# Optimization experiments

Measured on AMD Instinct MI355X. Metric: run time of the kernel, lower is better.

## Reference

```python
import jax, jax.numpy as jnp
import numpy as np

NEG_FILL = -100.0  # matches torch new_full(-100.0) init for scatter-amax


def reference(x, part_labels, parts_num=16):
    # x: (n, c, s, h, w) float; part_labels: (n, s, h, w) int in [0, parts_num)
    n, c, s, h, w = x.shape
    hw = h * w
    ns = n * s
    # (n s) c (h w)
    feat = jnp.transpose(x, (0, 2, 1, 3, 4)).reshape(ns, c, hw)
    labels = part_labels.reshape(ns, hw).astype(jnp.int32)

    b3 = jnp.arange(ns)[:, None, None]          # (ns,1,1)
    ch = jnp.arange(c)[None, :, None]            # (1,c,1)
    lbl3 = labels[:, None, :]                    # (ns,1,hw) -> broadcasts to (ns,c,hw)

    pooled_sum = jnp.zeros((ns, c, parts_num), x.dtype).at[b3, ch, lbl3].add(feat)
    b2 = jnp.arange(ns)[:, None]
    pooled_count = jnp.zeros((ns, parts_num), x.dtype).at[b2, labels].add(1.0)  # (ns,P)
    pooled_max = jnp.full((ns, c, parts_num), NEG_FILL, x.dtype).at[b3, ch, lbl3].max(feat)

    count = pooled_count[:, None, :]             # (ns,1,P)
    pooled_mean = pooled_sum / jnp.maximum(count, 1.0)
    pooled_max = jnp.where(count > 0, pooled_max, 0.0)
    pooled = pooled_mean + pooled_max            # (ns,c,P)
    # (n s) c p -> n c s p
    return jnp.transpose(pooled.reshape(n, s, c, parts_num), (0, 2, 1, 3))


def setup_inputs() -> dict:
    key = jax.random.key(0)
    k1, k2 = jax.random.split(key)
    n, c, s, h, w = 16, 256, 32, 16, 11
    parts_num = 16
    x = jax.random.normal(k1, (n, c, s, h, w), dtype=jnp.float32)
    part_labels = jax.random.randint(k2, (n, s, h, w), 0, parts_num, dtype=jnp.int64)
    return {"x": x, "part_labels": part_labels, "parts_num": parts_num}
```

## Files before the change

### kernel.cpp

```cpp
#include <hip/hip_runtime.h>


constexpr int C   = 256;
constexpr int S   = 32;
constexpr int HW  = 176;
constexpr int P   = 16;
constexpr int ROW = S * HW;
constexpr int GC  = 16;
constexpr int PITCH = 178;
constexpr int BCAP  = 64;
constexpr float NEG_FILL = -100.0f;

__device__ __forceinline__ void barrier_lgkm() {
    asm volatile("s_waitcnt lgkmcnt(0)\n\ts_barrier" ::: "memory");
}

__global__ __launch_bounds__(256) void hpp_kernel(
    const float* __restrict__ x,
    const int*   __restrict__ labels,
    float*       __restrict__ out)
{
    __shared__ float         tile[GC * PITCH];
    __shared__ unsigned char perm[P * BCAP];
    __shared__ int           cnt[P];

    const int tid = threadIdx.x;
    const int blk = blockIdx.x;
    const int ns  = blk >> 4, cg = blk & 15;
    const int n   = ns >> 5,  s  = ns & 31;

    const int* ln = labels + (size_t)ns * HW;
    int lab = 0;
    if (tid < HW) lab = ln[tid];

    const float* xb = x + (size_t)(n * C + cg * GC) * ROW + s * HW;
    const int f0 = tid, f1 = tid + 256, f2 = tid + 512;
    const int r0 = f0 / 44, j0 = f0 - r0 * 44;
    const int r1 = f1 / 44, j1 = f1 - r1 * 44;
    const int r2 = f2 / 44, j2 = f2 - r2 * 44;
    float4 v0 = *(const float4*)(xb + (size_t)r0 * ROW + j0 * 4);
    float4 v1 = *(const float4*)(xb + (size_t)r1 * ROW + j1 * 4);
    float4 v2 = make_float4(0.f, 0.f, 0.f, 0.f);
    const bool has2 = (f2 < GC * 44);
    if (has2) v2 = *(const float4*)(xb + (size_t)r2 * ROW + j2 * 4);

    ((unsigned*)perm)[tid] = 0u;
    if (tid < P) cnt[tid] = 0;
    barrier_lgkm();
    if (tid < HW) {
        int r = atomicAdd(&cnt[lab], 1);
        if (r < BCAP) perm[(lab << 6) + r] = (unsigned char)tid;
    }
    barrier_lgkm();

    {
        float2* t0 = (float2*)&tile[r0 * PITCH + j0 * 4];
        t0[0] = make_float2(v0.x, v0.y); t0[1] = make_float2(v0.z, v0.w);
        float2* t1 = (float2*)&tile[r1 * PITCH + j1 * 4];
        t1[0] = make_float2(v1.x, v1.y); t1[1] = make_float2(v1.z, v1.w);
        if (has2) {
            float2* t2 = (float2*)&tile[r2 * PITCH + j2 * 4];
            t2[0] = make_float2(v2.x, v2.y); t2[1] = make_float2(v2.z, v2.w);
        }
    }
    barrier_lgkm();

    const int p = tid >> 4, c = tid & 15;
    const int k = min(cnt[p], BCAP);
    const unsigned char* pp = &perm[p << 6];
    const float*         tc = &tile[c * PITCH];

    float s0 = 0.f, s1 = 0.f, m0 = NEG_FILL, m1 = NEG_FILL;
    const int kf = k & ~3;
    for (int j = 0; j < kf; j += 4) {
        unsigned u = *(const unsigned*)&pp[j];
        float a0 = tc[u & 0xFF];
        float a1 = tc[(u >> 8) & 0xFF];
        float a2 = tc[(u >> 16) & 0xFF];
        float a3 = tc[u >> 24];
        s0 += a0; m0 = fmaxf(m0, a0);
        s1 += a1; m1 = fmaxf(m1, a1);
        s0 += a2; m0 = fmaxf(m0, a2);
        s1 += a3; m1 = fmaxf(m1, a3);
    }
    if (kf < k) {
        unsigned u = *(const unsigned*)&pp[kf];
        float a0 = tc[u & 0xFF];
        float a1 = tc[(u >> 8) & 0xFF];
        float a2 = tc[(u >> 16) & 0xFF];
        s0 += a0; m0 = fmaxf(m0, a0);
        if (kf + 1 < k) { s1 += a1; m1 = fmaxf(m1, a1); }
        if (kf + 2 < k) { s0 += a2; m0 = fmaxf(m0, a2); }
    }

    float res = (k > 0) ? (s0 + s1) / (float)k + fmaxf(m0, m1) : 0.f;
    out[((size_t)(n * C + cg * GC + c) * S + s) * P + p] = res;
}

extern "C" void kernel_launch(void* const* d_in, const int* in_sizes, int n_in,
                              void* d_out, int out_size, void* d_ws, size_t ws_size,
                              hipStream_t stream) {
    const float* x      = (const float*)d_in[0];
    const int*   labels = (const int*)d_in[1];
    float*       out    = (float*)d_out;

    const int ns_total = in_sizes[1] / HW;
    const int nblk     = ns_total * (C / GC);
    hpp_kernel<<<nblk, 256, 0, stream>>>(x, labels, out);
}
```

Before: 135.5 us.

## Process two adjacent s slices per block with half the channels

Each block now covers 8 channels across two consecutive s positions instead of 16 channels at one s. Each channel's global read becomes a 352-float contiguous run, giving longer coalesced bursts, and two label rows are bucketed per block. The price is extra index arithmetic and a second set of part buckets in shared memory.

```diff
diff --git a/kernel.cpp b/kernel.cpp
--- a/kernel.cpp
+++ b/kernel.cpp
@@ -6,9 +6,11 @@
 constexpr int HW  = 176;
 constexpr int P   = 16;
 constexpr int ROW = S * HW;
-constexpr int GC  = 16;
+constexpr int GC  = 8;
+constexpr int NS2 = 2;
 constexpr int PITCH = 178;
 constexpr int BCAP  = 64;
+constexpr int PPITCH = 68;
 constexpr float NEG_FILL = -100.0f;
 
 __device__ __forceinline__ void barrier_lgkm() {
@@ -20,55 +22,65 @@
     const int*   __restrict__ labels,
     float*       __restrict__ out)
 {
-    __shared__ float         tile[GC * PITCH];
-    __shared__ unsigned char perm[P * BCAP];
-    __shared__ int           cnt[P];
+    __shared__ float         tile[GC * NS2 * PITCH];
+    __shared__ unsigned char perm[NS2 * P * PPITCH];
+    __shared__ int           cnt[NS2 * P];
 
     const int tid = threadIdx.x;
     const int blk = blockIdx.x;
-    const int ns  = blk >> 4, cg = blk & 15;
-    const int n   = ns >> 5,  s  = ns & 31;
+    const int nsp = blk >> 5, cg = blk & 31;
+    const int n   = nsp >> 4, sp = nsp & 15;
+    const int s   = sp * 2;
 
-    const int* ln = labels + (size_t)ns * HW;
-    int lab = 0;
-    if (tid < HW) lab = ln[tid];
+    const int* ln = labels + (size_t)(n * S + s) * HW;
+    int lab0 = 0, lab1 = 0;
+    if (tid < HW) { lab0 = ln[tid]; lab1 = ln[HW + tid]; }
 
     const float* xb = x + (size_t)(n * C + cg * GC) * ROW + s * HW;
     const int f0 = tid, f1 = tid + 256, f2 = tid + 512;
-    const int r0 = f0 / 44, j0 = f0 - r0 * 44;
-    const int r1 = f1 / 44, j1 = f1 - r1 * 44;
-    const int r2 = f2 / 44, j2 = f2 - r2 * 44;
+    const int r0 = f0 / 88, j0 = f0 - r0 * 88;
+    const int r1 = f1 / 88, j1 = f1 - r1 * 88;
+    const int r2 = f2 / 88, j2 = f2 - r2 * 88;
     float4 v0 = *(const float4*)(xb + (size_t)r0 * ROW + j0 * 4);
     float4 v1 = *(const float4*)(xb + (size_t)r1 * ROW + j1 * 4);
     float4 v2 = make_float4(0.f, 0.f, 0.f, 0.f);
-    const bool has2 = (f2 < GC * 44);
+    const bool has2 = (f2 < GC * 88);
     if (has2) v2 = *(const float4*)(xb + (size_t)r2 * ROW + j2 * 4);
 
-    ((unsigned*)perm)[tid] = 0u;
-    if (tid < P) cnt[tid] = 0;
+    if (tid < NS2 * P) cnt[tid] = 0;
     barrier_lgkm();
     if (tid < HW) {
-        int r = atomicAdd(&cnt[lab], 1);
-        if (r < BCAP) perm[(lab << 6) + r] = (unsigned char)tid;
+        int a = atomicAdd(&cnt[lab0], 1);
+        if (a < BCAP) perm[lab0 * PPITCH + a] = (unsigned char)tid;
+        int b = atomicAdd(&cnt[P + lab1], 1);
+        if (b < BCAP) perm[P * PPITCH + lab1 * PPITCH + b] = (unsigned char)tid;
     }
     barrier_lgkm();
 
     {
-        float2* t0 = (float2*)&tile[r0 * PITCH + j0 * 4];
+        const int q0 = j0 * 4, s20 = (q0 >= HW), h0 = q0 - s20 * HW;
+        float2* t0 = (float2*)&tile[(r0 * 2 + s20) * PITCH + h0];
         t0[0] = make_float2(v0.x, v0.y); t0[1] = make_float2(v0.z, v0.w);
-        float2* t1 = (float2*)&tile[r1 * PITCH + j1 * 4];
+
+        const int q1 = j1 * 4, s21 = (q1 >= HW), h1 = q1 - s21 * HW;
+        float2* t1 = (float2*)&tile[(r1 * 2 + s21) * PITCH + h1];
         t1[0] = make_float2(v1.x, v1.y); t1[1] = make_float2(v1.z, v1.w);
+
         if (has2) {
-            float2* t2 = (float2*)&tile[r2 * PITCH + j2 * 4];
+            const int q2 = j2 * 4, s22 = (q2 >= HW), h2 = q2 - s22 * HW;
+            float2* t2 = (float2*)&tile[(r2 * 2 + s22) * PITCH + h2];
             t2[0] = make_float2(v2.x, v2.y); t2[1] = make_float2(v2.z, v2.w);
         }
     }
     barrier_lgkm();
 
-    const int p = tid >> 4, c = tid & 15;
-    const int k = min(cnt[p], BCAP);
-    const unsigned char* pp = &perm[p << 6];
-    const float*         tc = &tile[c * PITCH];
+    const int p   = tid >> 4;
+    const int low = tid & 15;
+    const int sp2 = low & 1;
+    const int c   = low >> 1;
+    const int k   = min(cnt[sp2 * P + p], BCAP);
+    const unsigned char* pp = &perm[(sp2 * P + p) * PPITCH];
+    const float*         tc = &tile[low * PITCH];
 
     float s0 = 0.f, s1 = 0.f, m0 = NEG_FILL, m1 = NEG_FILL;
     const int kf = k & ~3;
@@ -94,7 +106,7 @@
     }
 
     float res = (k > 0) ? (s0 + s1) / (float)k + fmaxf(m0, m1) : 0.f;
-    out[((size_t)(n * C + cg * GC + c) * S + s) * P + p] = res;
+    out[((size_t)(n * C + cg * GC + c) * S + (s + sp2)) * P + p] = res;
 }
 
 extern "C" void kernel_launch(void* const* d_in, const int* in_sizes, int n_in,
@@ -105,6 +117,6 @@
     float*       out    = (float*)d_out;
 
     const int ns_total = in_sizes[1] / HW;
-    const int nblk     = ns_total * (C / GC);
+    const int nblk     = (ns_total / NS2) * (C / GC);
     hpp_kernel<<<nblk, 256, 0, stream>>>(x, labels, out);
 }
```

New measurement: 136.1 us. About the same (+0.5%).

## Precompute label buckets in a separate kernel and scatter x into part-sorted tiles

Applied to the files above, without the earlier changes.

Adds a bucket kernel that computes, for each (n,s) frame, each pixel's position in part-sorted order, plus per-part base offsets and counts, and writes these to workspace. The main kernel now handles one (n,c) row with all 32 frames. It scatters the loaded float4s into shared memory in part-sorted order so each part becomes a contiguous run that can be reduced with float4 loads, and the output row is written contiguously. This removes the per-block label bucketing and the byte-index gather, at the cost of an extra launch and scattered shared-memory writes. The old kernel is kept as a fallback when the workspace is too small.

```diff
diff --git a/kernel.cpp b/kernel.cpp
--- a/kernel.cpp
+++ b/kernel.cpp
@@ -6,21 +6,143 @@
 constexpr int HW  = 176;
 constexpr int P   = 16;
 constexpr int ROW = S * HW;
-constexpr int GC  = 16;
-constexpr int PITCH = 178;
-constexpr int BCAP  = 64;
+constexpr int PITCH = 180;
 constexpr float NEG_FILL = -100.0f;
 
 __device__ __forceinline__ void barrier_lgkm() {
     asm volatile("s_waitcnt lgkmcnt(0)\n\ts_barrier" ::: "memory");
 }
 
-__global__ __launch_bounds__(256) void hpp_kernel(
+__global__ __launch_bounds__(256) void bucket_kernel(
+    const int* __restrict__ labels,
+    unsigned*  __restrict__ pm,
+    unsigned*  __restrict__ pk)
+{
+    __shared__ int cnt[P];
+    __shared__ int base[P];
+    __shared__ __align__(4) unsigned char posmap[HW];
+
+    const int tid = threadIdx.x;
+    const int ns  = blockIdx.x;
+
+    int lab = 0, r = 0;
+    if (tid < HW) lab = labels[(size_t)ns * HW + tid];
+    if (tid < P)  cnt[tid] = 0;
+    __syncthreads();
+    if (tid < HW) r = atomicAdd(&cnt[lab], 1);
+    __syncthreads();
+    if (tid < P) {
+        int acc = 0;
+        for (int q = 0; q < tid; ++q) acc += cnt[q];
+        base[tid] = acc;
+    }
+    __syncthreads();
+    if (tid < HW) posmap[tid] = (unsigned char)(base[lab] + r);
+    __syncthreads();
+    if (tid < HW / 4) pm[(size_t)ns * 44 + tid] = ((const unsigned*)posmap)[tid];
+    if (tid < P)      pk[(size_t)ns * P + tid] =
+                          ((unsigned)base[tid] << 8) | (unsigned)cnt[tid];
+}
+
+__global__ __launch_bounds__(256) void hpp_main(
+    const float*    __restrict__ x,
+    const unsigned* __restrict__ pm,
+    const unsigned* __restrict__ pk,
+    float*          __restrict__ out)
+{
+    __shared__ float tile[S * PITCH];
+
+    const int tid = threadIdx.x;
+    const int blk = blockIdx.x;
+    const int n   = blk >> 8, c = blk & 255;
+
+    const unsigned* pmn = pm + (size_t)n * S * 44;
+    const unsigned* pkn = pk + (size_t)n * S * P;
+    unsigned w0 = pmn[tid];
+    unsigned w1 = pmn[tid + 256];
+    unsigned w2 = pmn[tid + 512];
+    unsigned w3 = pmn[tid + 768];
+    unsigned w4 = pmn[tid + 1024];
+    const bool has5 = (tid < 1408 - 1280);
+    unsigned w5 = 0; if (has5) w5 = pmn[tid + 1280];
+    unsigned q0 = pkn[tid];
+    unsigned q1 = pkn[tid + 256];
+
+    const float4* xr = (const float4*)(x + (size_t)(n * C + c) * ROW);
+    float4 v0 = xr[tid];
+    float4 v1 = xr[tid + 256];
+    float4 v2 = xr[tid + 512];
+    float4 v3 = xr[tid + 768];
+    float4 v4 = xr[tid + 1024];
+    float4 v5 = make_float4(0.f, 0.f, 0.f, 0.f);
+    if (has5) v5 = xr[tid + 1280];
+
+    {
+#define SCAT(J, W, V)                                                      \
+        {                                                                  \
+            const int s_ = (J) / 44;                                       \
+            float* t_ = &tile[s_ * PITCH];                                 \
+            t_[(W) & 0xFF] = (V).x;  t_[((W) >> 8) & 0xFF] = (V).y;        \
+            t_[((W) >> 16) & 0xFF] = (V).z;  t_[(W) >> 24] = (V).w;        \
+        }
+        SCAT(tid,        w0, v0)
+        SCAT(tid + 256,  w1, v1)
+        SCAT(tid + 512,  w2, v2)
+        SCAT(tid + 768,  w3, v3)
+        SCAT(tid + 1024, w4, v4)
+        if (has5) SCAT(tid + 1280, w5, v5)
+#undef SCAT
+    }
+    barrier_lgkm();
+
+    float res[2];
+    #pragma unroll
+    for (int o = 0; o < 2; ++o) {
+        const unsigned w = o ? q1 : q0;
+        const int k   = (int)(w & 0xFF);
+        int off       = (int)(w >> 8);
+        const int idx = tid + o * 256;
+        const float* tc = &tile[(idx >> 4) * PITCH];
+
+        float s0 = 0.f, s1 = 0.f, m0 = NEG_FILL, m1 = NEG_FILL;
+        int rem = k;
+        int h = (4 - (off & 3)) & 3; if (h > rem) h = rem;
+        if (h > 0) { float a = tc[off];     s0 += a; m0 = fmaxf(m0, a); }
+        if (h > 1) { float a = tc[off + 1]; s1 += a; m1 = fmaxf(m1, a); }
+        if (h > 2) { float a = tc[off + 2]; s0 += a; m0 = fmaxf(m0, a); }
+        off += h; rem -= h;
+        int n4 = rem >> 2;
+        for (int i = 0; i < n4; ++i) {
+            float4 q = *(const float4*)&tc[off];
+            s0 += q.x; m0 = fmaxf(m0, q.x);
+            s1 += q.y; m1 = fmaxf(m1, q.y);
+            s0 += q.z; m0 = fmaxf(m0, q.z);
+            s1 += q.w; m1 = fmaxf(m1, q.w);
+            off += 4;
+        }
+        rem &= 3;
+        if (rem > 0) { float a = tc[off];     s0 += a; m0 = fmaxf(m0, a); }
+        if (rem > 1) { float a = tc[off + 1]; s1 += a; m1 = fmaxf(m1, a); }
+        if (rem > 2) { float a = tc[off + 2]; s0 += a; m0 = fmaxf(m0, a); }
+
+        res[o] = (k > 0) ? (s0 + s1) / (float)k + fmaxf(m0, m1) : 0.f;
+    }
+
+    float* op = out + (size_t)(n * C + c) * (S * P);
+    op[tid]       = res[0];
+    op[tid + 256] = res[1];
+}
+
+constexpr int GC_F  = 16;
+constexpr int PIT_F = 178;
+constexpr int BCAP  = 64;
+
+__global__ __launch_bounds__(256) void hpp_fallback(
     const float* __restrict__ x,
     const int*   __restrict__ labels,
     float*       __restrict__ out)
 {
-    __shared__ float         tile[GC * PITCH];
+    __shared__ float         tile[GC_F * PIT_F];
     __shared__ unsigned char perm[P * BCAP];
     __shared__ int           cnt[P];
 
@@ -33,7 +155,7 @@
     int lab = 0;
     if (tid < HW) lab = ln[tid];
 
-    const float* xb = x + (size_t)(n * C + cg * GC) * ROW + s * HW;
+    const float* xb = x + (size_t)(n * C + cg * GC_F) * ROW + s * HW;
     const int f0 = tid, f1 = tid + 256, f2 = tid + 512;
     const int r0 = f0 / 44, j0 = f0 - r0 * 44;
     const int r1 = f1 / 44, j1 = f1 - r1 * 44;
@@ -41,7 +163,7 @@
     float4 v0 = *(const float4*)(xb + (size_t)r0 * ROW + j0 * 4);
     float4 v1 = *(const float4*)(xb + (size_t)r1 * ROW + j1 * 4);
     float4 v2 = make_float4(0.f, 0.f, 0.f, 0.f);
-    const bool has2 = (f2 < GC * 44);
+    const bool has2 = (f2 < GC_F * 44);
     if (has2) v2 = *(const float4*)(xb + (size_t)r2 * ROW + j2 * 4);
 
     ((unsigned*)perm)[tid] = 0u;
@@ -52,14 +174,13 @@
         if (r < BCAP) perm[(lab << 6) + r] = (unsigned char)tid;
     }
     barrier_lgkm();
-
     {
-        float2* t0 = (float2*)&tile[r0 * PITCH + j0 * 4];
+        float2* t0 = (float2*)&tile[r0 * PIT_F + j0 * 4];
         t0[0] = make_float2(v0.x, v0.y); t0[1] = make_float2(v0.z, v0.w);
-        float2* t1 = (float2*)&tile[r1 * PITCH + j1 * 4];
+        float2* t1 = (float2*)&tile[r1 * PIT_F + j1 * 4];
         t1[0] = make_float2(v1.x, v1.y); t1[1] = make_float2(v1.z, v1.w);
         if (has2) {
-            float2* t2 = (float2*)&tile[r2 * PITCH + j2 * 4];
+            float2* t2 = (float2*)&tile[r2 * PIT_F + j2 * 4];
             t2[0] = make_float2(v2.x, v2.y); t2[1] = make_float2(v2.z, v2.w);
         }
     }
@@ -68,7 +189,7 @@
     const int p = tid >> 4, c = tid & 15;
     const int k = min(cnt[p], BCAP);
     const unsigned char* pp = &perm[p << 6];
-    const float*         tc = &tile[c * PITCH];
+    const float*         tc = &tile[c * PIT_F];
 
     float s0 = 0.f, s1 = 0.f, m0 = NEG_FILL, m1 = NEG_FILL;
     const int kf = k & ~3;
@@ -94,7 +215,7 @@
     }
 
     float res = (k > 0) ? (s0 + s1) / (float)k + fmaxf(m0, m1) : 0.f;
-    out[((size_t)(n * C + cg * GC + c) * S + s) * P + p] = res;
+    out[((size_t)(n * C + cg * GC_F + c) * S + s) * P + p] = res;
 }
 
 extern "C" void kernel_launch(void* const* d_in, const int* in_sizes, int n_in,
@@ -105,6 +226,16 @@
     float*       out    = (float*)d_out;
 
     const int ns_total = in_sizes[1] / HW;
-    const int nblk     = ns_total * (C / GC);
-    hpp_kernel<<<nblk, 256, 0, stream>>>(x, labels, out);
-}
+    const size_t pm_bytes = (size_t)ns_total * 44 * 4;
+    const size_t pk_bytes = (size_t)ns_total * P * 4;
+
+    if (ws_size >= pm_bytes + pk_bytes) {
+        unsigned* pm = (unsigned*)d_ws;
+        unsigned* pk = (unsigned*)((char*)d_ws + pm_bytes);
+        bucket_kernel<<<ns_total, 256, 0, stream>>>(labels, pm, pk);
+        const int nblk = (ns_total / S) * C;
+        hpp_main<<<nblk, 256, 0, stream>>>(x, pm, pk, out);
+    } else {
+        hpp_fallback<<<ns_total * (C / GC_F), 256, 0, stream>>>(x, labels, out);
+    }
+}
```

Measured after the change: 137.9 us. About the same (+1.8%).
